# Performance work log

Measured on AMD Instinct MI355X. Metric: run time of the kernel, lower is better.

The kernel has to match this reference:

```python
import jax, jax.numpy as jnp
import numpy as np

N_NODES = 100000
N_EDGES = 1600000
IN, HID, OUT = 32, 32, 16


def setup_inputs() -> dict:
    key = jax.random.key(0)
    ks = jax.random.split(key, 8)
    return {
        "features": jax.random.normal(ks[0], (N_NODES, IN), dtype=jnp.float32),
        "src": jax.random.randint(ks[1], (N_EDGES,), 0, N_NODES, dtype=jnp.int32),
        "dst": jax.random.randint(ks[2], (N_EDGES,), 0, N_NODES, dtype=jnp.int32),
        "edge_weight": jax.random.uniform(ks[3], (N_EDGES,), dtype=jnp.float32),
        "W1": jax.random.normal(ks[4], (IN, HID), dtype=jnp.float32) * 0.1,
        "b1": jnp.zeros((HID,), dtype=jnp.float32),
        "W2": jax.random.normal(ks[5], (HID, OUT), dtype=jnp.float32) * 0.1,
        "b2": jnp.zeros((OUT,), dtype=jnp.float32),
    }


def _graph_conv(h, W, b, src, dst, edge_weight, norm_src, norm_dst, n):
    # DGL GraphConv, norm='both', with edge_weight (u_mul_e aggregation)
    h = h * norm_src[:, None]          # out-degree^-0.5 on source side
    h = h @ W                          # dense transform (tiny GEMM)
    m = h[src] * edge_weight[:, None]  # gather + edge weighting  [E, d]
    agg = jax.ops.segment_sum(m, dst, num_segments=n)  # scatter-add SpMM
    return agg * norm_dst[:, None] + b # in-degree^-0.5 + bias


def reference(features, src, dst, edge_weight, W1, b1, W2, b2):
    n = features.shape[0]
    ones_e = jnp.ones_like(edge_weight)
    deg_out = jnp.clip(jax.ops.segment_sum(ones_e, src, num_segments=n), 1.0)
    deg_in = jnp.clip(jax.ops.segment_sum(ones_e, dst, num_segments=n), 1.0)
    norm_src = deg_out ** -0.5
    norm_dst = deg_in ** -0.5
    h = _graph_conv(features, W1, b1, src, dst, edge_weight, norm_src, norm_dst, n)
    h = jax.nn.relu(h)
    # dropout is identity in eval mode
    h = _graph_conv(h, W2, b2, src, dst, edge_weight, norm_src, norm_dst, n)
    return h
```

## Files before the change

### kernel.cpp

```cpp
#include <hip/hip_runtime.h>
#include <hip/hip_fp16.h>


#define NB   391
#define CAPB 5504
#define EPB  4096

__device__ __forceinline__ long nt_load_i64(const long* p) {
    return __builtin_nontemporal_load(p);
}

__global__ __launch_bounds__(512) void partition_kernel(
        const int* __restrict__ src, const int* __restrict__ dst,
        const float* __restrict__ ew,
        int* __restrict__ g_cur_d, int* __restrict__ g_cur_s,
        int2* __restrict__ pack_part, unsigned char* __restrict__ src_part, int m) {
    __shared__ int hist_d[NB], hist_s[NB];
    __shared__ int lbase_d[NB], lbase_s[NB];
    __shared__ int gbase_d[NB], gbase_s[NB];
    __shared__ int cur_d[NB], cur_s[NB];
    __shared__ int sc[2][512];
    __shared__ long stage[EPB];
    __shared__ unsigned short dbuck[EPB];
    __shared__ unsigned char  sstage[EPB];
    __shared__ unsigned short sbuck[EPB];
    int t = threadIdx.x;
    for (int i = t; i < NB; i += 512) {
        hist_d[i] = 0; hist_s[i] = 0; cur_d[i] = 0; cur_s[i] = 0;
    }
    __syncthreads();
    int base_e = blockIdx.x * EPB;
    int total = m - base_e; if (total > EPB) total = EPB;
    int es[8], ed[8]; float wv[8];
#pragma unroll
    for (int k = 0; k < 8; k++) {
        int e = base_e + k * 512 + t;
        if (e < m) { es[k] = src[e]; ed[k] = dst[e]; wv[k] = ew[e]; }
        else ed[k] = -1;
    }
#pragma unroll
    for (int k = 0; k < 8; k++) {
        if (ed[k] >= 0) {
            atomicAdd(&hist_d[ed[k] >> 8], 1);
            atomicAdd(&hist_s[es[k] >> 8], 1);
        }
    }
    __syncthreads();
    if (t < 512) sc[0][t] = (t < NB) ? hist_d[t] : 0;
    __syncthreads();
    int pp = 0;
    for (int off = 1; off < 512; off <<= 1) {
        sc[1 - pp][t] = sc[pp][t] + (t >= off ? sc[pp][t - off] : 0);
        __syncthreads();
        pp ^= 1;
    }
    for (int i = t; i < NB; i += 512) lbase_d[i] = sc[pp][i] - hist_d[i];
    __syncthreads();
    sc[0][t] = (t < NB) ? hist_s[t] : 0;
    __syncthreads();
    pp = 0;
    for (int off = 1; off < 512; off <<= 1) {
        sc[1 - pp][t] = sc[pp][t] + (t >= off ? sc[pp][t - off] : 0);
        __syncthreads();
        pp ^= 1;
    }
    for (int i = t; i < NB; i += 512) lbase_s[i] = sc[pp][i] - hist_s[i];
    __syncthreads();
    for (int i = t; i < NB; i += 512) {
        int c = hist_d[i];
        gbase_d[i] = i * CAPB + (c ? atomicAdd(&g_cur_d[i], c) : 0);
        c = hist_s[i];
        gbase_s[i] = i * CAPB + (c ? atomicAdd(&g_cur_s[i], c) : 0);
    }
    __syncthreads();
#pragma unroll
    for (int k = 0; k < 8; k++) {
        if (ed[k] >= 0) {
            int d = ed[k], s = es[k];
            int bd = d >> 8;
            int r = atomicAdd(&cur_d[bd], 1);
            int pos = lbase_d[bd] + r;
            stage[pos] = (long)(unsigned int)(s | ((d & 255) << 20)) |
                         ((long)__float_as_int(wv[k]) << 32);
            dbuck[pos] = (unsigned short)bd;
            int bs = s >> 8;
            int rs = atomicAdd(&cur_s[bs], 1);
            int ps = lbase_s[bs] + rs;
            sstage[ps] = (unsigned char)(s & 255);
            sbuck[ps] = (unsigned short)bs;
        }
    }
    __syncthreads();
    long* packl = (long*)pack_part;
    for (int i = t; i < total; i += 512) {
        int b = dbuck[i];
        packl[(size_t)gbase_d[b] + (i - lbase_d[b])] = stage[i];
    }
    for (int i = t; i < total; i += 512) {
        int b = sbuck[i];
        src_part[(size_t)gbase_s[b] + (i - lbase_s[b])] = sstage[i];
    }
}

__global__ __launch_bounds__(1024) void csr_kernel(
                           const int2* __restrict__ pack_part,
                           const unsigned char* __restrict__ src_part,
                           const int* __restrict__ g_cur_d, const int* __restrict__ g_cur_s,
                           const float* __restrict__ feat, const float* __restrict__ W1,
                           int2* __restrict__ csr, int2* __restrict__ rs_cnt,
                           float* __restrict__ norm_src, float* __restrict__ norm_dst,
                           __half* __restrict__ h1, int n) {
    __shared__ int cnt[256];
    __shared__ int rowx[256];
    __shared__ int cur[256];
    __shared__ int cnt_s[256];
    __shared__ float nsrc[256];
    __shared__ float sW1[1024];
    extern __shared__ int2 stage[];
    int t = threadIdx.x, b = blockIdx.x;
    if (t < 256) { cnt[t] = 0; cur[t] = 0; cnt_s[t] = 0; }
    sW1[t] = W1[t];
    __syncthreads();
    int count = g_cur_d[b]; if (count > CAPB) count = CAPB;
    int count_s = g_cur_s[b]; if (count_s > CAPB) count_s = CAPB;
    const int2* p = pack_part + (size_t)b * CAPB;
    const unsigned char* sp = src_part + (size_t)b * CAPB;
    for (int e = t; e < count; e += 1024) atomicAdd(&cnt[p[e].x >> 20], 1);
    for (int e = t; e < count_s; e += 1024) atomicAdd(&cnt_s[sp[e]], 1);
    __syncthreads();
    if (t < 256) {
        int node = b * 256 + t;
        if (node < n) {
            int cs = cnt_s[t];
            float ns = rsqrtf((float)(cs > 1 ? cs : 1));
            nsrc[t] = ns;
            norm_src[node] = ns;
        } else nsrc[t] = 0.0f;
    }
    int c0 = 0;
    if (t < 256) { c0 = cnt[t]; rowx[t] = c0; }
    __syncthreads();
    for (int off = 1; off < 256; off <<= 1) {
        int v = 0;
        if (t < 256 && t >= off) v = rowx[t - off];
        __syncthreads();
        if (t < 256) rowx[t] += v;
        __syncthreads();
    }
    if (t < 256) {
        int excl = rowx[t] - c0;
        rowx[t] = excl;
        int node = b * 256 + t;
        if (node < n) {
            rs_cnt[node] = make_int2(b * CAPB + excl, c0);
            norm_dst[node] = rsqrtf((float)(c0 > 1 ? c0 : 1));
        }
    }
    __syncthreads();
    for (int e = t; e < count; e += 1024) {
        int2 v = p[e];
        int dl = v.x >> 20;
        int r = atomicAdd(&cur[dl], 1);
        stage[rowx[dl] + r] = make_int2(v.x & 0x1FFFF, v.y);
    }
    __syncthreads();
    int2* outp = csr + (size_t)b * CAPB;
    for (int e = t; e < count; e += 1024) outp[e] = stage[e];
    __syncthreads();
    float* sF = (float*)stage;
    int node0 = b * 256;
    int lim = n - node0; if (lim > 256) lim = 256; if (lim < 0) lim = 0;
    for (int o = t; o < lim * 32; o += 1024) {
        int i = o >> 5, k = o & 31;
        sF[o] = feat[(size_t)(node0 + i) * 32 + k] * nsrc[i];
    }
    __syncthreads();
    for (int o = t; o < lim * 32; o += 1024) {
        int i = o >> 5, col = o & 31;
        float acc = 0.0f;
#pragma unroll
        for (int k = 0; k < 32; k++) acc += sF[i * 32 + k] * sW1[k * 32 + col];
        h1[(size_t)(node0 + i) * 32 + col] = __float2half(acc);
    }
}

__global__ void gather1_fused_kernel(const __half* __restrict__ h1, const int2* __restrict__ csr,
                                     const int2* __restrict__ rs_cnt,
                                     const float* __restrict__ norm_src, const float* __restrict__ norm_dst,
                                     const float* __restrict__ W2, const float* __restrict__ b1,
                                     __half* __restrict__ h2, int n) {
    __shared__ float sW2[32 * 16];
    __shared__ float sB1[32];
    __shared__ float sX[4][8][32];
    int t = threadIdx.x;
    for (int i = t; i < 512; i += 256) sW2[i] = W2[i];
    if (t < 32) sB1[t] = b1[t];
    __syncthreads();
    int w = t >> 6, lane = t & 63;
    int q = lane >> 3;
    int dq = lane & 7;
    int node = (blockIdx.x * 4 + w) * 8 + q;
    bool valid = node < n;
    int2 rc = valid ? rs_cnt[node] : make_int2(0, 0);
    long base = rc.x;
    int c = rc.y;
    const float2* tv = (const float2*)h1;
    const long* csrl = (const long*)csr;
    float a00=0,a01=0,a02=0,a03=0, a10=0,a11=0,a12=0,a13=0;
    float a20=0,a21=0,a22=0,a23=0, a30=0,a31=0,a32=0,a33=0;
    int j = 0;
    for (; j + 3 < c; j += 4) {
        long q0 = nt_load_i64(csrl + base + j);
        long q1 = nt_load_i64(csrl + base + j + 1);
        long q2 = nt_load_i64(csrl + base + j + 2);
        long q3 = nt_load_i64(csrl + base + j + 3);
        float2 r0 = tv[(size_t)((int)q0 & 0xFFFFF) * 8 + dq];
        float2 r1 = tv[(size_t)((int)q1 & 0xFFFFF) * 8 + dq];
        float2 r2 = tv[(size_t)((int)q2 & 0xFFFFF) * 8 + dq];
        float2 r3 = tv[(size_t)((int)q3 & 0xFFFFF) * 8 + dq];
        float w0 = __int_as_float((int)(q0 >> 32)), w1 = __int_as_float((int)(q1 >> 32));
        float w2 = __int_as_float((int)(q2 >> 32)), w3 = __int_as_float((int)(q3 >> 32));
        float2 l0 = __half22float2(*(__half2*)&r0.x), h0 = __half22float2(*(__half2*)&r0.y);
        float2 l1 = __half22float2(*(__half2*)&r1.x), h1v = __half22float2(*(__half2*)&r1.y);
        float2 l2 = __half22float2(*(__half2*)&r2.x), h2v = __half22float2(*(__half2*)&r2.y);
        float2 l3 = __half22float2(*(__half2*)&r3.x), h3v = __half22float2(*(__half2*)&r3.y);
        a00 += l0.x * w0; a01 += l0.y * w0; a02 += h0.x * w0; a03 += h0.y * w0;
        a10 += l1.x * w1; a11 += l1.y * w1; a12 += h1v.x * w1; a13 += h1v.y * w1;
        a20 += l2.x * w2; a21 += l2.y * w2; a22 += h2v.x * w2; a23 += h2v.y * w2;
        a30 += l3.x * w3; a31 += l3.y * w3; a32 += h3v.x * w3; a33 += h3v.y * w3;
    }
    for (; j < c; j++) {
        long qq = nt_load_i64(csrl + base + j);
        float2 r = tv[(size_t)((int)qq & 0xFFFFF) * 8 + dq];
        float ww = __int_as_float((int)(qq >> 32));
        float2 l = __half22float2(*(__half2*)&r.x), h = __half22float2(*(__half2*)&r.y);
        a00 += l.x * ww; a01 += l.y * ww; a02 += h.x * ww; a03 += h.y * ww;
    }
    float s0 = (a00 + a10) + (a20 + a30);
    float s1 = (a01 + a11) + (a21 + a31);
    float s2 = (a02 + a12) + (a22 + a32);
    float s3 = (a03 + a13) + (a23 + a33);
    if (valid) {
        float nd = norm_dst[node], ns = norm_src[node];
        int d0 = 4 * dq;
        sX[w][q][d0]     = fmaxf(s0 * nd + sB1[d0],     0.0f) * ns;
        sX[w][q][d0 + 1] = fmaxf(s1 * nd + sB1[d0 + 1], 0.0f) * ns;
        sX[w][q][d0 + 2] = fmaxf(s2 * nd + sB1[d0 + 2], 0.0f) * ns;
        sX[w][q][d0 + 3] = fmaxf(s3 * nd + sB1[d0 + 3], 0.0f) * ns;
    }
    if (valid) {
        float o0 = 0.0f, o1 = 0.0f;
        int c0 = 2 * dq, c1 = 2 * dq + 1;
#pragma unroll
        for (int k = 0; k < 32; k++) {
            float x = sX[w][q][k];
            o0 += x * sW2[k * 16 + c0];
            o1 += x * sW2[k * 16 + c1];
        }
        ((__half2*)h2)[(size_t)node * 8 + dq] = __floats2half2_rn(o0, o1);
    }
}

__global__ void gather2_kernel(const __half* __restrict__ h2, const int2* __restrict__ csr,
                               const int2* __restrict__ rs_cnt,
                               const float* __restrict__ norm_dst, const float* __restrict__ b2,
                               float* __restrict__ out, int n) {
    int t = threadIdx.x;
    int w = t >> 6, lane = t & 63;
    int q = lane >> 2;
    int dq = lane & 3;
    int node = (blockIdx.x * 4 + w) * 16 + q;
    bool valid = node < n;
    int2 rc = valid ? rs_cnt[node] : make_int2(0, 0);
    long base = rc.x;
    int c = rc.y;
    const float2* tv = (const float2*)h2;
    const long* csrl = (const long*)csr;
    float a00=0,a01=0,a02=0,a03=0, a10=0,a11=0,a12=0,a13=0;
    float a20=0,a21=0,a22=0,a23=0, a30=0,a31=0,a32=0,a33=0;
    int j = 0;
    for (; j + 3 < c; j += 4) {
        long q0 = nt_load_i64(csrl + base + j);
        long q1 = nt_load_i64(csrl + base + j + 1);
        long q2 = nt_load_i64(csrl + base + j + 2);
        long q3 = nt_load_i64(csrl + base + j + 3);
        float2 r0 = tv[(size_t)((int)q0 & 0xFFFFF) * 4 + dq];
        float2 r1 = tv[(size_t)((int)q1 & 0xFFFFF) * 4 + dq];
        float2 r2 = tv[(size_t)((int)q2 & 0xFFFFF) * 4 + dq];
        float2 r3 = tv[(size_t)((int)q3 & 0xFFFFF) * 4 + dq];
        float w0 = __int_as_float((int)(q0 >> 32)), w1 = __int_as_float((int)(q1 >> 32));
        float w2 = __int_as_float((int)(q2 >> 32)), w3 = __int_as_float((int)(q3 >> 32));
        float2 l0 = __half22float2(*(__half2*)&r0.x), h0 = __half22float2(*(__half2*)&r0.y);
        float2 l1 = __half22float2(*(__half2*)&r1.x), h1v = __half22float2(*(__half2*)&r1.y);
        float2 l2 = __half22float2(*(__half2*)&r2.x), h2v = __half22float2(*(__half2*)&r2.y);
        float2 l3 = __half22float2(*(__half2*)&r3.x), h3v = __half22float2(*(__half2*)&r3.y);
        a00 += l0.x * w0; a01 += l0.y * w0; a02 += h0.x * w0; a03 += h0.y * w0;
        a10 += l1.x * w1; a11 += l1.y * w1; a12 += h1v.x * w1; a13 += h1v.y * w1;
        a20 += l2.x * w2; a21 += l2.y * w2; a22 += h2v.x * w2; a23 += h2v.y * w2;
        a30 += l3.x * w3; a31 += l3.y * w3; a32 += h3v.x * w3; a33 += h3v.y * w3;
    }
    for (; j < c; j++) {
        long qq = nt_load_i64(csrl + base + j);
        float2 r = tv[(size_t)((int)qq & 0xFFFFF) * 4 + dq];
        float ww = __int_as_float((int)(qq >> 32));
        float2 l = __half22float2(*(__half2*)&r.x), h = __half22float2(*(__half2*)&r.y);
        a00 += l.x * ww; a01 += l.y * ww; a02 += h.x * ww; a03 += h.y * ww;
    }
    if (valid) {
        float nd = norm_dst[node];
        int d0 = 4 * dq;
        float4 o;
        o.x = ((a00 + a10) + (a20 + a30)) * nd + b2[d0];
        o.y = ((a01 + a11) + (a21 + a31)) * nd + b2[d0 + 1];
        o.z = ((a02 + a12) + (a22 + a32)) * nd + b2[d0 + 2];
        o.w = ((a03 + a13) + (a23 + a33)) * nd + b2[d0 + 3];
        ((float4*)out)[(size_t)node * 4 + dq] = o;
    }
}

extern "C" void kernel_launch(void* const* d_in, const int* in_sizes, int n_in,
                              void* d_out, int out_size, void* d_ws, size_t ws_size,
                              hipStream_t stream) {
    const float* feat = (const float*)d_in[0];
    const int*   src  = (const int*)d_in[1];
    const int*   dst  = (const int*)d_in[2];
    const float* ew   = (const float*)d_in[3];
    const float* W1   = (const float*)d_in[4];
    const float* b1   = (const float*)d_in[5];
    const float* W2   = (const float*)d_in[6];
    const float* b2   = (const float*)d_in[7];
    float* out = (float*)d_out;

    const int n = in_sizes[0] / 32;
    const int m = in_sizes[1];

    char* wsb = (char*)d_ws;
    int2*   pack_part = (int2*)wsb;
    int2*   csr       = pack_part + (size_t)NB * CAPB;
    __half* h1        = (__half*)(csr + (size_t)NB * CAPB);
    __half* h2        = h1 + 32 * (size_t)n;
    float*  norm_src  = (float*)(h2 + 16 * (size_t)n);
    float*  norm_dst  = norm_src + n;
    int2*   rs_cnt    = (int2*)(norm_dst + n);
    int*    g_cur_d   = (int*)(rs_cnt + n);
    int*    g_cur_s   = g_cur_d + NB;
    unsigned char* src_part = (unsigned char*)(g_cur_s + NB);

    hipMemsetAsync(g_cur_d, 0, 2 * NB * sizeof(int), stream);

    partition_kernel<<<(m + EPB - 1) / EPB, 512, 0, stream>>>(src, dst, ew, g_cur_d, g_cur_s,
                                                              pack_part, src_part, m);
    csr_kernel<<<NB, 1024, CAPB * sizeof(int2), stream>>>(pack_part, src_part, g_cur_d, g_cur_s,
                                                          feat, W1, csr, rs_cnt,
                                                          norm_src, norm_dst, h1, n);
    gather1_fused_kernel<<<(n + 31) / 32, 256, 0, stream>>>(h1, csr, rs_cnt,
                                                            norm_src, norm_dst, W2, b1, h2, n);
    gather2_kernel<<<(n + 63) / 64, 256, 0, stream>>>(h2, csr, rs_cnt, norm_dst, b2, out, n);
}
```

Baseline: 186.9 us.

## Compute source degrees with global atomics and replace block scans with wave shuffles

Drops the second source-side bucket partition (histogram, scan, staging and the src_part scatter). Out-degrees are now counted with direct global atomicAdd into a per-node deg_src array, which csr_kernel reads. The shared-memory prefix scans are replaced with wavefront shuffle scans, csr_kernel keeps the first packed edges in registers instead of reading them twice, and the feature transform is vectorized with float4 loads, padded shared rows and half2 stores. The cost is 1.6M scattered global atomics and a larger memset covering n ints.

Measured after the change: 237.6 us. 27.2% more time.

```diff
diff --git a/kernel.cpp b/kernel.cpp
--- a/kernel.cpp
+++ b/kernel.cpp
@@ -13,21 +13,18 @@
 __global__ __launch_bounds__(512) void partition_kernel(
         const int* __restrict__ src, const int* __restrict__ dst,
         const float* __restrict__ ew,
-        int* __restrict__ g_cur_d, int* __restrict__ g_cur_s,
-        int2* __restrict__ pack_part, unsigned char* __restrict__ src_part, int m) {
-    __shared__ int hist_d[NB], hist_s[NB];
-    __shared__ int lbase_d[NB], lbase_s[NB];
-    __shared__ int gbase_d[NB], gbase_s[NB];
-    __shared__ int cur_d[NB], cur_s[NB];
-    __shared__ int sc[2][512];
+        int* __restrict__ g_cur_d, int* __restrict__ deg_src,
+        int2* __restrict__ pack_part, int m) {
+    __shared__ int hist_d[NB];
+    __shared__ int lbase_d[NB];
+    __shared__ int gbase_d[NB];
+    __shared__ int cur_d[NB];
+    __shared__ int woff[8];
     __shared__ long stage[EPB];
     __shared__ unsigned short dbuck[EPB];
-    __shared__ unsigned char  sstage[EPB];
-    __shared__ unsigned short sbuck[EPB];
     int t = threadIdx.x;
-    for (int i = t; i < NB; i += 512) {
-        hist_d[i] = 0; hist_s[i] = 0; cur_d[i] = 0; cur_s[i] = 0;
-    }
+    int lane = t & 63, w = t >> 6;
+    for (int i = t; i < NB; i += 512) { hist_d[i] = 0; cur_d[i] = 0; }
     __syncthreads();
     int base_e = blockIdx.x * EPB;
     int total = m - base_e; if (total > EPB) total = EPB;
@@ -42,35 +39,34 @@
     for (int k = 0; k < 8; k++) {
         if (ed[k] >= 0) {
             atomicAdd(&hist_d[ed[k] >> 8], 1);
-            atomicAdd(&hist_s[es[k] >> 8], 1);
-        }
-    }
-    __syncthreads();
-    if (t < 512) sc[0][t] = (t < NB) ? hist_d[t] : 0;
-    __syncthreads();
-    int pp = 0;
-    for (int off = 1; off < 512; off <<= 1) {
-        sc[1 - pp][t] = sc[pp][t] + (t >= off ? sc[pp][t - off] : 0);
-        __syncthreads();
-        pp ^= 1;
-    }
-    for (int i = t; i < NB; i += 512) lbase_d[i] = sc[pp][i] - hist_d[i];
-    __syncthreads();
-    sc[0][t] = (t < NB) ? hist_s[t] : 0;
-    __syncthreads();
-    pp = 0;
-    for (int off = 1; off < 512; off <<= 1) {
-        sc[1 - pp][t] = sc[pp][t] + (t >= off ? sc[pp][t - off] : 0);
-        __syncthreads();
-        pp ^= 1;
-    }
-    for (int i = t; i < NB; i += 512) lbase_s[i] = sc[pp][i] - hist_s[i];
-    __syncthreads();
+            atomicAdd(&deg_src[es[k]], 1);
+        }
+    }
+    __syncthreads();
+    int hv = (t < NB) ? hist_d[t] : 0;
+    int v = hv;
+#pragma unroll
+    for (int off = 1; off < 64; off <<= 1) {
+        int u = __shfl_up(v, off, 64);
+        if (lane >= off) v += u;
+    }
+    if (lane == 63) woff[w] = v;
+    __syncthreads();
+    if (t < 64) {
+        int s = (t < 8) ? woff[t] : 0;
+        int orig = s;
+#pragma unroll
+        for (int off = 1; off < 8; off <<= 1) {
+            int u = __shfl_up(s, off, 64);
+            if (lane >= off) s += u;
+        }
+        if (t < 8) woff[t] = s - orig;
+    }
+    __syncthreads();
+    if (t < NB) lbase_d[t] = v + woff[w] - hv;
     for (int i = t; i < NB; i += 512) {
         int c = hist_d[i];
         gbase_d[i] = i * CAPB + (c ? atomicAdd(&g_cur_d[i], c) : 0);
-        c = hist_s[i];
-        gbase_s[i] = i * CAPB + (c ? atomicAdd(&g_cur_s[i], c) : 0);
     }
     __syncthreads();
 #pragma unroll
@@ -83,11 +79,6 @@
             stage[pos] = (long)(unsigned int)(s | ((d & 255) << 20)) |
                          ((long)__float_as_int(wv[k]) << 32);
             dbuck[pos] = (unsigned short)bd;
-            int bs = s >> 8;
-            int rs = atomicAdd(&cur_s[bs], 1);
-            int ps = lbase_s[bs] + rs;
-            sstage[ps] = (unsigned char)(s & 255);
-            sbuck[ps] = (unsigned short)bs;
         }
     }
     __syncthreads();
@@ -96,16 +87,11 @@
         int b = dbuck[i];
         packl[(size_t)gbase_d[b] + (i - lbase_d[b])] = stage[i];
     }
-    for (int i = t; i < total; i += 512) {
-        int b = sbuck[i];
-        src_part[(size_t)gbase_s[b] + (i - lbase_s[b])] = sstage[i];
-    }
 }
 
 __global__ __launch_bounds__(1024) void csr_kernel(
                            const int2* __restrict__ pack_part,
-                           const unsigned char* __restrict__ src_part,
-                           const int* __restrict__ g_cur_d, const int* __restrict__ g_cur_s,
+                           const int* __restrict__ g_cur_d, const int* __restrict__ deg_src,
                            const float* __restrict__ feat, const float* __restrict__ W1,
                            int2* __restrict__ csr, int2* __restrict__ rs_cnt,
                            float* __restrict__ norm_src, float* __restrict__ norm_dst,
@@ -113,51 +99,65 @@
     __shared__ int cnt[256];
     __shared__ int rowx[256];
     __shared__ int cur[256];
-    __shared__ int cnt_s[256];
     __shared__ float nsrc[256];
     __shared__ float sW1[1024];
     extern __shared__ int2 stage[];
     int t = threadIdx.x, b = blockIdx.x;
-    if (t < 256) { cnt[t] = 0; cur[t] = 0; cnt_s[t] = 0; }
+    if (t < 256) { cnt[t] = 0; cur[t] = 0; }
     sW1[t] = W1[t];
     __syncthreads();
     int count = g_cur_d[b]; if (count > CAPB) count = CAPB;
-    int count_s = g_cur_s[b]; if (count_s > CAPB) count_s = CAPB;
     const int2* p = pack_part + (size_t)b * CAPB;
-    const unsigned char* sp = src_part + (size_t)b * CAPB;
-    for (int e = t; e < count; e += 1024) atomicAdd(&cnt[p[e].x >> 20], 1);
-    for (int e = t; e < count_s; e += 1024) atomicAdd(&cnt_s[sp[e]], 1);
-    __syncthreads();
+    int2 pk[4];
+#pragma unroll
+    for (int u = 0; u < 4; u++) {
+        int e = t + u * 1024;
+        if (e < count) { pk[u] = p[e]; atomicAdd(&cnt[pk[u].x >> 20], 1); }
+    }
+    for (int e = t + 4096; e < count; e += 1024)
+        atomicAdd(&cnt[p[e].x >> 20], 1);
+    __syncthreads();
+    if (t < 64) {
+        int c0 = cnt[t * 4], c1 = cnt[t * 4 + 1], c2 = cnt[t * 4 + 2], c3 = cnt[t * 4 + 3];
+        int tot = c0 + c1 + c2 + c3;
+        int incl = tot;
+#pragma unroll
+        for (int off = 1; off < 64; off <<= 1) {
+            int u = __shfl_up(incl, off, 64);
+            if (t >= off) incl += u;
+        }
+        int excl = incl - tot;
+        rowx[t * 4]     = excl;
+        rowx[t * 4 + 1] = excl + c0;
+        rowx[t * 4 + 2] = excl + c0 + c1;
+        rowx[t * 4 + 3] = excl + c0 + c1 + c2;
+    }
+    __syncthreads();
+    int node0 = b * 256;
     if (t < 256) {
-        int node = b * 256 + t;
+        int node = node0 + t;
         if (node < n) {
-            int cs = cnt_s[t];
-            float ns = rsqrtf((float)(cs > 1 ? cs : 1));
+            int c0 = cnt[t];
+            rs_cnt[node] = make_int2(b * CAPB + rowx[t], c0);
+            norm_dst[node] = rsqrtf((float)(c0 > 1 ? c0 : 1));
+            int ds = deg_src[node];
+            float ns = rsqrtf((float)(ds > 1 ? ds : 1));
             nsrc[t] = ns;
             norm_src[node] = ns;
         } else nsrc[t] = 0.0f;
     }
-    int c0 = 0;
-    if (t < 256) { c0 = cnt[t]; rowx[t] = c0; }
-    __syncthreads();
-    for (int off = 1; off < 256; off <<= 1) {
-        int v = 0;
-        if (t < 256 && t >= off) v = rowx[t - off];
-        __syncthreads();
-        if (t < 256) rowx[t] += v;
-        __syncthreads();
-    }
-    if (t < 256) {
-        int excl = rowx[t] - c0;
-        rowx[t] = excl;
-        int node = b * 256 + t;
-        if (node < n) {
-            rs_cnt[node] = make_int2(b * CAPB + excl, c0);
-            norm_dst[node] = rsqrtf((float)(c0 > 1 ? c0 : 1));
-        }
-    }
-    __syncthreads();
-    for (int e = t; e < count; e += 1024) {
+    __syncthreads();
+#pragma unroll
+    for (int u = 0; u < 4; u++) {
+        int e = t + u * 1024;
+        if (e < count) {
+            int2 v = pk[u];
+            int dl = v.x >> 20;
+            int r = atomicAdd(&cur[dl], 1);
+            stage[rowx[dl] + r] = make_int2(v.x & 0x1FFFF, v.y);
+        }
+    }
+    for (int e = t + 4096; e < count; e += 1024) {
         int2 v = p[e];
         int dl = v.x >> 20;
         int r = atomicAdd(&cur[dl], 1);
@@ -168,19 +168,27 @@
     for (int e = t; e < count; e += 1024) outp[e] = stage[e];
     __syncthreads();
     float* sF = (float*)stage;
-    int node0 = b * 256;
     int lim = n - node0; if (lim > 256) lim = 256; if (lim < 0) lim = 0;
-    for (int o = t; o < lim * 32; o += 1024) {
-        int i = o >> 5, k = o & 31;
-        sF[o] = feat[(size_t)(node0 + i) * 32 + k] * nsrc[i];
-    }
-    __syncthreads();
-    for (int o = t; o < lim * 32; o += 1024) {
-        int i = o >> 5, col = o & 31;
-        float acc = 0.0f;
-#pragma unroll
-        for (int k = 0; k < 32; k++) acc += sF[i * 32 + k] * sW1[k * 32 + col];
-        h1[(size_t)(node0 + i) * 32 + col] = __float2half(acc);
+    const float4* f4 = (const float4*)feat;
+    for (int o = t; o < lim * 8; o += 1024) {
+        int i = o >> 3, k4 = o & 7;
+        float4 vv = f4[(size_t)node0 * 8 + o];
+        float ns = nsrc[i];
+        vv.x *= ns; vv.y *= ns; vv.z *= ns; vv.w *= ns;
+        ((float4*)(sF + i * 36))[k4] = vv;
+    }
+    __syncthreads();
+    __half2* h1v = (__half2*)h1;
+    for (int o = t; o < lim * 16; o += 1024) {
+        int i = o >> 4, cp = o & 15;
+        float a0 = 0.0f, a1 = 0.0f;
+#pragma unroll
+        for (int k = 0; k < 32; k++) {
+            float x = sF[i * 36 + k];
+            a0 += x * sW1[k * 32 + 2 * cp];
+            a1 += x * sW1[k * 32 + 2 * cp + 1];
+        }
+        h1v[(size_t)(node0 + i) * 16 + cp] = __floats2half2_rn(a0, a1);
     }
 }
 
@@ -191,7 +199,7 @@
                                      __half* __restrict__ h2, int n) {
     __shared__ float sW2[32 * 16];
     __shared__ float sB1[32];
-    __shared__ float sX[4][8][32];
+    __shared__ float sX[4][8][33];
     int t = threadIdx.x;
     for (int i = t; i < 512; i += 256) sW2[i] = W2[i];
     if (t < 32) sB1[t] = b1[t];
@@ -343,14 +351,13 @@
     float*  norm_dst  = norm_src + n;
     int2*   rs_cnt    = (int2*)(norm_dst + n);
     int*    g_cur_d   = (int*)(rs_cnt + n);
-    int*    g_cur_s   = g_cur_d + NB;
-    unsigned char* src_part = (unsigned char*)(g_cur_s + NB);
-
-    hipMemsetAsync(g_cur_d, 0, 2 * NB * sizeof(int), stream);
-
-    partition_kernel<<<(m + EPB - 1) / EPB, 512, 0, stream>>>(src, dst, ew, g_cur_d, g_cur_s,
-                                                              pack_part, src_part, m);
-    csr_kernel<<<NB, 1024, CAPB * sizeof(int2), stream>>>(pack_part, src_part, g_cur_d, g_cur_s,
+    int*    deg_src   = g_cur_d + NB;
+
+    hipMemsetAsync(g_cur_d, 0, (NB + n) * sizeof(int), stream);
+
+    partition_kernel<<<(m + EPB - 1) / EPB, 512, 0, stream>>>(src, dst, ew, g_cur_d, deg_src,
+                                                              pack_part, m);
+    csr_kernel<<<NB, 1024, CAPB * sizeof(int2), stream>>>(pack_part, g_cur_d, deg_src,
                                                           feat, W1, csr, rs_cnt,
                                                           norm_src, norm_dst, h1, n);
     gather1_fused_kernel<<<(n + 31) / 32, 256, 0, stream>>>(h1, csr, rs_cnt,
```

## Replace CSR build and per-node gathers with bucketed LDS atomic accumulation

Applied to the files above, without the earlier changes.

Drops the per-bucket CSR sort. The two aggregation kernels now read the destination-bucketed edge partitions directly and accumulate each 256-node bucket in shared memory with float atomics. The degree-based norm_dst is computed inside the first gather, and the partition kernel's block scans are rewritten as wave shuffle scans. This removes the CSR write/read pass and the rs_cnt indirection, but only 391 blocks are launched and the many LDS atomics may contend on high-degree nodes.

New measurement: 637.9 us. 241% more time.

```diff
diff --git a/kernel.cpp b/kernel.cpp
--- a/kernel.cpp
+++ b/kernel.cpp
@@ -5,10 +5,6 @@
 #define NB   391
 #define CAPB 5504
 #define EPB  4096
-
-__device__ __forceinline__ long nt_load_i64(const long* p) {
-    return __builtin_nontemporal_load(p);
-}
 
 __global__ __launch_bounds__(512) void partition_kernel(
         const int* __restrict__ src, const int* __restrict__ dst,
@@ -19,12 +15,12 @@
     __shared__ int lbase_d[NB], lbase_s[NB];
     __shared__ int gbase_d[NB], gbase_s[NB];
     __shared__ int cur_d[NB], cur_s[NB];
-    __shared__ int sc[2][512];
+    __shared__ int woffd[8], woffs[8];
     __shared__ long stage[EPB];
     __shared__ unsigned short dbuck[EPB];
     __shared__ unsigned char  sstage[EPB];
     __shared__ unsigned short sbuck[EPB];
-    int t = threadIdx.x;
+    int t = threadIdx.x, lane = t & 63, w = t >> 6;
     for (int i = t; i < NB; i += 512) {
         hist_d[i] = 0; hist_s[i] = 0; cur_d[i] = 0; cur_s[i] = 0;
     }
@@ -46,26 +42,34 @@
         }
     }
     __syncthreads();
-    if (t < 512) sc[0][t] = (t < NB) ? hist_d[t] : 0;
-    __syncthreads();
-    int pp = 0;
-    for (int off = 1; off < 512; off <<= 1) {
-        sc[1 - pp][t] = sc[pp][t] + (t >= off ? sc[pp][t - off] : 0);
-        __syncthreads();
-        pp ^= 1;
-    }
-    for (int i = t; i < NB; i += 512) lbase_d[i] = sc[pp][i] - hist_d[i];
-    __syncthreads();
-    sc[0][t] = (t < NB) ? hist_s[t] : 0;
-    __syncthreads();
-    pp = 0;
-    for (int off = 1; off < 512; off <<= 1) {
-        sc[1 - pp][t] = sc[pp][t] + (t >= off ? sc[pp][t - off] : 0);
-        __syncthreads();
-        pp ^= 1;
-    }
-    for (int i = t; i < NB; i += 512) lbase_s[i] = sc[pp][i] - hist_s[i];
-    __syncthreads();
+    int hvd = (t < NB) ? hist_d[t] : 0;
+    int hvs = (t < NB) ? hist_s[t] : 0;
+    int vd = hvd, vs = hvs;
+#pragma unroll
+    for (int off = 1; off < 64; off <<= 1) {
+        int ud = __shfl_up(vd, off, 64);
+        int us = __shfl_up(vs, off, 64);
+        if (lane >= off) { vd += ud; vs += us; }
+    }
+    if (lane == 63) { woffd[w] = vd; woffs[w] = vs; }
+    __syncthreads();
+    if (t < 64) {
+        int sd = (t < 8) ? woffd[t] : 0;
+        int ss = (t < 8) ? woffs[t] : 0;
+        int od = sd, os = ss;
+#pragma unroll
+        for (int off = 1; off < 8; off <<= 1) {
+            int ud = __shfl_up(sd, off, 64);
+            int us = __shfl_up(ss, off, 64);
+            if (lane >= off) { sd += ud; ss += us; }
+        }
+        if (t < 8) { woffd[t] = sd - od; woffs[t] = ss - os; }
+    }
+    __syncthreads();
+    if (t < NB) {
+        lbase_d[t] = vd + woffd[w] - hvd;
+        lbase_s[t] = vs + woffs[w] - hvs;
+    }
     for (int i = t; i < NB; i += 512) {
         int c = hist_d[i];
         gbase_d[i] = i * CAPB + (c ? atomicAdd(&g_cur_d[i], c) : 0);
@@ -102,219 +106,172 @@
     }
 }
 
-__global__ __launch_bounds__(1024) void csr_kernel(
-                           const int2* __restrict__ pack_part,
-                           const unsigned char* __restrict__ src_part,
-                           const int* __restrict__ g_cur_d, const int* __restrict__ g_cur_s,
-                           const float* __restrict__ feat, const float* __restrict__ W1,
-                           int2* __restrict__ csr, int2* __restrict__ rs_cnt,
-                           float* __restrict__ norm_src, float* __restrict__ norm_dst,
-                           __half* __restrict__ h1, int n) {
-    __shared__ int cnt[256];
-    __shared__ int rowx[256];
-    __shared__ int cur[256];
+__global__ __launch_bounds__(1024) void transform1_kernel(
+        const unsigned char* __restrict__ src_part, const int* __restrict__ g_cur_s,
+        const float* __restrict__ feat, const float* __restrict__ W1,
+        float* __restrict__ norm_src, __half* __restrict__ h1, int n) {
     __shared__ int cnt_s[256];
     __shared__ float nsrc[256];
     __shared__ float sW1[1024];
-    extern __shared__ int2 stage[];
+    __shared__ __align__(16) float sF[256 * 36];
     int t = threadIdx.x, b = blockIdx.x;
-    if (t < 256) { cnt[t] = 0; cur[t] = 0; cnt_s[t] = 0; }
+    if (t < 256) cnt_s[t] = 0;
     sW1[t] = W1[t];
     __syncthreads();
-    int count = g_cur_d[b]; if (count > CAPB) count = CAPB;
     int count_s = g_cur_s[b]; if (count_s > CAPB) count_s = CAPB;
-    const int2* p = pack_part + (size_t)b * CAPB;
     const unsigned char* sp = src_part + (size_t)b * CAPB;
-    for (int e = t; e < count; e += 1024) atomicAdd(&cnt[p[e].x >> 20], 1);
     for (int e = t; e < count_s; e += 1024) atomicAdd(&cnt_s[sp[e]], 1);
     __syncthreads();
+    int node0 = b * 256;
     if (t < 256) {
-        int node = b * 256 + t;
+        int node = node0 + t;
         if (node < n) {
-            int cs = cnt_s[t];
-            float ns = rsqrtf((float)(cs > 1 ? cs : 1));
+            int ds = cnt_s[t];
+            float ns = rsqrtf((float)(ds > 1 ? ds : 1));
             nsrc[t] = ns;
             norm_src[node] = ns;
         } else nsrc[t] = 0.0f;
     }
-    int c0 = 0;
-    if (t < 256) { c0 = cnt[t]; rowx[t] = c0; }
-    __syncthreads();
-    for (int off = 1; off < 256; off <<= 1) {
-        int v = 0;
-        if (t < 256 && t >= off) v = rowx[t - off];
-        __syncthreads();
-        if (t < 256) rowx[t] += v;
-        __syncthreads();
-    }
-    if (t < 256) {
-        int excl = rowx[t] - c0;
-        rowx[t] = excl;
-        int node = b * 256 + t;
-        if (node < n) {
-            rs_cnt[node] = make_int2(b * CAPB + excl, c0);
-            norm_dst[node] = rsqrtf((float)(c0 > 1 ? c0 : 1));
-        }
-    }
-    __syncthreads();
-    for (int e = t; e < count; e += 1024) {
-        int2 v = p[e];
-        int dl = v.x >> 20;
-        int r = atomicAdd(&cur[dl], 1);
-        stage[rowx[dl] + r] = make_int2(v.x & 0x1FFFF, v.y);
-    }
-    __syncthreads();
-    int2* outp = csr + (size_t)b * CAPB;
-    for (int e = t; e < count; e += 1024) outp[e] = stage[e];
-    __syncthreads();
-    float* sF = (float*)stage;
+    __syncthreads();
+    int lim = n - node0; if (lim > 256) lim = 256; if (lim < 0) lim = 0;
+    const float4* f4 = (const float4*)feat;
+    for (int o = t; o < lim * 8; o += 1024) {
+        int i = o >> 3, k4 = o & 7;
+        float4 vv = f4[(size_t)node0 * 8 + o];
+        float ns = nsrc[i];
+        vv.x *= ns; vv.y *= ns; vv.z *= ns; vv.w *= ns;
+        ((float4*)(sF + i * 36))[k4] = vv;
+    }
+    __syncthreads();
+    __half2* h1v = (__half2*)h1;
+    for (int o = t; o < lim * 16; o += 1024) {
+        int i = o >> 4, cp = o & 15;
+        float a0 = 0.0f, a1 = 0.0f;
+#pragma unroll
+        for (int k = 0; k < 32; k++) {
+            float x = sF[i * 36 + k];
+            a0 += x * sW1[k * 32 + 2 * cp];
+            a1 += x * sW1[k * 32 + 2 * cp + 1];
+        }
+        h1v[(size_t)(node0 + i) * 16 + cp] = __floats2half2_rn(a0, a1);
+    }
+}
+
+__global__ __launch_bounds__(1024) void gather1_kernel(
+        const int2* __restrict__ pack_part, const int* __restrict__ g_cur_d,
+        const __half* __restrict__ h1, const float* __restrict__ norm_src,
+        const float* __restrict__ W2, const float* __restrict__ b1,
+        float* __restrict__ norm_dst, __half* __restrict__ h2, int n) {
+    __shared__ float acc[256 * 33];
+    __shared__ int cnt[256];
+    __shared__ float sW2[512];
+    __shared__ float sB1[32];
+    __shared__ float sndv[256], snsv[256];
+    int t = threadIdx.x, b = blockIdx.x;
+    for (int i = t; i < 256 * 33; i += 1024) acc[i] = 0.0f;
+    if (t < 256) cnt[t] = 0;
+    if (t < 512) sW2[t] = W2[t];
+    else if (t < 544) sB1[t - 512] = b1[t - 512];
+    __syncthreads();
+    int count = g_cur_d[b]; if (count > CAPB) count = CAPB;
+    const int2* p = pack_part + (size_t)b * CAPB;
+    const float4* h1f4 = (const float4*)h1;
+    int eq = t >> 2, q = t & 3;
+    for (int e0 = 0; e0 < count; e0 += 256) {
+        int e = e0 + eq;
+        if (e < count) {
+            int2 v = p[e];
+            int s  = v.x & 0x1FFFF;
+            int dl = (v.x >> 20) & 255;
+            float wgt = __int_as_float(v.y);
+            if (q == 0) atomicAdd(&cnt[dl], 1);
+            float4 r = h1f4[(size_t)s * 4 + q];
+            float* ap = acc + dl * 33 + 8 * q;
+            const __half2* hp = (const __half2*)&r;
+#pragma unroll
+            for (int j = 0; j < 4; j++) {
+                float2 f = __half22float2(hp[j]);
+                atomicAdd(ap + 2 * j,     f.x * wgt);
+                atomicAdd(ap + 2 * j + 1, f.y * wgt);
+            }
+        }
+    }
+    __syncthreads();
     int node0 = b * 256;
     int lim = n - node0; if (lim > 256) lim = 256; if (lim < 0) lim = 0;
+    if (t < 256) {
+        int c0 = cnt[t];
+        float nd = rsqrtf((float)(c0 > 1 ? c0 : 1));
+        sndv[t] = nd;
+        snsv[t] = (t < lim) ? norm_src[node0 + t] : 0.0f;
+        if (t < lim) norm_dst[node0 + t] = nd;
+    }
+    __syncthreads();
     for (int o = t; o < lim * 32; o += 1024) {
         int i = o >> 5, k = o & 31;
-        sF[o] = feat[(size_t)(node0 + i) * 32 + k] * nsrc[i];
-    }
-    __syncthreads();
-    for (int o = t; o < lim * 32; o += 1024) {
-        int i = o >> 5, col = o & 31;
-        float acc = 0.0f;
-#pragma unroll
-        for (int k = 0; k < 32; k++) acc += sF[i * 32 + k] * sW1[k * 32 + col];
-        h1[(size_t)(node0 + i) * 32 + col] = __float2half(acc);
-    }
-}
-
-__global__ void gather1_fused_kernel(const __half* __restrict__ h1, const int2* __restrict__ csr,
-                                     const int2* __restrict__ rs_cnt,
-                                     const float* __restrict__ norm_src, const float* __restrict__ norm_dst,
-                                     const float* __restrict__ W2, const float* __restrict__ b1,
-                                     __half* __restrict__ h2, int n) {
-    __shared__ float sW2[32 * 16];
-    __shared__ float sB1[32];
-    __shared__ float sX[4][8][32];
-    int t = threadIdx.x;
-    for (int i = t; i < 512; i += 256) sW2[i] = W2[i];
-    if (t < 32) sB1[t] = b1[t];
-    __syncthreads();
-    int w = t >> 6, lane = t & 63;
-    int q = lane >> 3;
-    int dq = lane & 7;
-    int node = (blockIdx.x * 4 + w) * 8 + q;
-    bool valid = node < n;
-    int2 rc = valid ? rs_cnt[node] : make_int2(0, 0);
-    long base = rc.x;
-    int c = rc.y;
-    const float2* tv = (const float2*)h1;
-    const long* csrl = (const long*)csr;
-    float a00=0,a01=0,a02=0,a03=0, a10=0,a11=0,a12=0,a13=0;
-    float a20=0,a21=0,a22=0,a23=0, a30=0,a31=0,a32=0,a33=0;
-    int j = 0;
-    for (; j + 3 < c; j += 4) {
-        long q0 = nt_load_i64(csrl + base + j);
-        long q1 = nt_load_i64(csrl + base + j + 1);
-        long q2 = nt_load_i64(csrl + base + j + 2);
-        long q3 = nt_load_i64(csrl + base + j + 3);
-        float2 r0 = tv[(size_t)((int)q0 & 0xFFFFF) * 8 + dq];
-        float2 r1 = tv[(size_t)((int)q1 & 0xFFFFF) * 8 + dq];
-        float2 r2 = tv[(size_t)((int)q2 & 0xFFFFF) * 8 + dq];
-        float2 r3 = tv[(size_t)((int)q3 & 0xFFFFF) * 8 + dq];
-        float w0 = __int_as_float((int)(q0 >> 32)), w1 = __int_as_float((int)(q1 >> 32));
-        float w2 = __int_as_float((int)(q2 >> 32)), w3 = __int_as_float((int)(q3 >> 32));
-        float2 l0 = __half22float2(*(__half2*)&r0.x), h0 = __half22float2(*(__half2*)&r0.y);
-        float2 l1 = __half22float2(*(__half2*)&r1.x), h1v = __half22float2(*(__half2*)&r1.y);
-        float2 l2 = __half22float2(*(__half2*)&r2.x), h2v = __half22float2(*(__half2*)&r2.y);
-        float2 l3 = __half22float2(*(__half2*)&r3.x), h3v = __half22float2(*(__half2*)&r3.y);
-        a00 += l0.x * w0; a01 += l0.y * w0; a02 += h0.x * w0; a03 += h0.y * w0;
-        a10 += l1.x * w1; a11 += l1.y * w1; a12 += h1v.x * w1; a13 += h1v.y * w1;
-        a20 += l2.x * w2; a21 += l2.y * w2; a22 += h2v.x * w2; a23 += h2v.y * w2;
-        a30 += l3.x * w3; a31 += l3.y * w3; a32 += h3v.x * w3; a33 += h3v.y * w3;
-    }
-    for (; j < c; j++) {
-        long qq = nt_load_i64(csrl + base + j);
-        float2 r = tv[(size_t)((int)qq & 0xFFFFF) * 8 + dq];
-        float ww = __int_as_float((int)(qq >> 32));
-        float2 l = __half22float2(*(__half2*)&r.x), h = __half22float2(*(__half2*)&r.y);
-        a00 += l.x * ww; a01 += l.y * ww; a02 += h.x * ww; a03 += h.y * ww;
-    }
-    float s0 = (a00 + a10) + (a20 + a30);
-    float s1 = (a01 + a11) + (a21 + a31);
-    float s2 = (a02 + a12) + (a22 + a32);
-    float s3 = (a03 + a13) + (a23 + a33);
-    if (valid) {
-        float nd = norm_dst[node], ns = norm_src[node];
-        int d0 = 4 * dq;
-        sX[w][q][d0]     = fmaxf(s0 * nd + sB1[d0],     0.0f) * ns;
-        sX[w][q][d0 + 1] = fmaxf(s1 * nd + sB1[d0 + 1], 0.0f) * ns;
-        sX[w][q][d0 + 2] = fmaxf(s2 * nd + sB1[d0 + 2], 0.0f) * ns;
-        sX[w][q][d0 + 3] = fmaxf(s3 * nd + sB1[d0 + 3], 0.0f) * ns;
-    }
-    if (valid) {
-        float o0 = 0.0f, o1 = 0.0f;
-        int c0 = 2 * dq, c1 = 2 * dq + 1;
+        float x = fmaxf(acc[i * 33 + k] * sndv[i] + sB1[k], 0.0f) * snsv[i];
+        acc[i * 33 + k] = x;
+    }
+    __syncthreads();
+    __half2* h2v = (__half2*)h2;
+    for (int o = t; o < lim * 8; o += 1024) {
+        int i = o >> 3, cp = o & 7;
+        float a0 = 0.0f, a1 = 0.0f;
 #pragma unroll
         for (int k = 0; k < 32; k++) {
-            float x = sX[w][q][k];
-            o0 += x * sW2[k * 16 + c0];
-            o1 += x * sW2[k * 16 + c1];
-        }
-        ((__half2*)h2)[(size_t)node * 8 + dq] = __floats2half2_rn(o0, o1);
-    }
-}
-
-__global__ void gather2_kernel(const __half* __restrict__ h2, const int2* __restrict__ csr,
-                               const int2* __restrict__ rs_cnt,
-                               const float* __restrict__ norm_dst, const float* __restrict__ b2,
-                               float* __restrict__ out, int n) {
-    int t = threadIdx.x;
-    int w = t >> 6, lane = t & 63;
-    int q = lane >> 2;
-    int dq = lane & 3;
-    int node = (blockIdx.x * 4 + w) * 16 + q;
-    bool valid = node < n;
-    int2 rc = valid ? rs_cnt[node] : make_int2(0, 0);
-    long base = rc.x;
-    int c = rc.y;
-    const float2* tv = (const float2*)h2;
-    const long* csrl = (const long*)csr;
-    float a00=0,a01=0,a02=0,a03=0, a10=0,a11=0,a12=0,a13=0;
-    float a20=0,a21=0,a22=0,a23=0, a30=0,a31=0,a32=0,a33=0;
-    int j = 0;
-    for (; j + 3 < c; j += 4) {
-        long q0 = nt_load_i64(csrl + base + j);
-        long q1 = nt_load_i64(csrl + base + j + 1);
-        long q2 = nt_load_i64(csrl + base + j + 2);
-        long q3 = nt_load_i64(csrl + base + j + 3);
-        float2 r0 = tv[(size_t)((int)q0 & 0xFFFFF) * 4 + dq];
-        float2 r1 = tv[(size_t)((int)q1 & 0xFFFFF) * 4 + dq];
-        float2 r2 = tv[(size_t)((int)q2 & 0xFFFFF) * 4 + dq];
-        float2 r3 = tv[(size_t)((int)q3 & 0xFFFFF) * 4 + dq];
-        float w0 = __int_as_float((int)(q0 >> 32)), w1 = __int_as_float((int)(q1 >> 32));
-        float w2 = __int_as_float((int)(q2 >> 32)), w3 = __int_as_float((int)(q3 >> 32));
-        float2 l0 = __half22float2(*(__half2*)&r0.x), h0 = __half22float2(*(__half2*)&r0.y);
-        float2 l1 = __half22float2(*(__half2*)&r1.x), h1v = __half22float2(*(__half2*)&r1.y);
-        float2 l2 = __half22float2(*(__half2*)&r2.x), h2v = __half22float2(*(__half2*)&r2.y);
-        float2 l3 = __half22float2(*(__half2*)&r3.x), h3v = __half22float2(*(__half2*)&r3.y);
-        a00 += l0.x * w0; a01 += l0.y * w0; a02 += h0.x * w0; a03 += h0.y * w0;
-        a10 += l1.x * w1; a11 += l1.y * w1; a12 += h1v.x * w1; a13 += h1v.y * w1;
-        a20 += l2.x * w2; a21 += l2.y * w2; a22 += h2v.x * w2; a23 += h2v.y * w2;
-        a30 += l3.x * w3; a31 += l3.y * w3; a32 += h3v.x * w3; a33 += h3v.y * w3;
-    }
-    for (; j < c; j++) {
-        long qq = nt_load_i64(csrl + base + j);
-        float2 r = tv[(size_t)((int)qq & 0xFFFFF) * 4 + dq];
-        float ww = __int_as_float((int)(qq >> 32));
-        float2 l = __half22float2(*(__half2*)&r.x), h = __half22float2(*(__half2*)&r.y);
-        a00 += l.x * ww; a01 += l.y * ww; a02 += h.x * ww; a03 += h.y * ww;
-    }
-    if (valid) {
-        float nd = norm_dst[node];
-        int d0 = 4 * dq;
-        float4 o;
-        o.x = ((a00 + a10) + (a20 + a30)) * nd + b2[d0];
-        o.y = ((a01 + a11) + (a21 + a31)) * nd + b2[d0 + 1];
-        o.z = ((a02 + a12) + (a22 + a32)) * nd + b2[d0 + 2];
-        o.w = ((a03 + a13) + (a23 + a33)) * nd + b2[d0 + 3];
-        ((float4*)out)[(size_t)node * 4 + dq] = o;
+            float x = acc[i * 33 + k];
+            a0 += x * sW2[k * 16 + 2 * cp];
+            a1 += x * sW2[k * 16 + 2 * cp + 1];
+        }
+        h2v[(size_t)(node0 + i) * 8 + cp] = __floats2half2_rn(a0, a1);
+    }
+}
+
+__global__ __launch_bounds__(1024) void gather2_kernel(
+        const int2* __restrict__ pack_part, const int* __restrict__ g_cur_d,
+        const __half* __restrict__ h2, const float* __restrict__ norm_dst,
+        const float* __restrict__ b2, float* __restrict__ out, int n) {
+    __shared__ __align__(16) float acc[256 * 20];
+    __shared__ float sB2[16];
+    int t = threadIdx.x, b = blockIdx.x;
+    for (int i = t; i < 256 * 20; i += 1024) acc[i] = 0.0f;
+    if (t < 16) sB2[t] = b2[t];
+    __syncthreads();
+    int count = g_cur_d[b]; if (count > CAPB) count = CAPB;
+    const int2* p = pack_part + (size_t)b * CAPB;
+    const float4* h2f4 = (const float4*)h2;
+    int eq = t >> 1, q = t & 1;
+    for (int e0 = 0; e0 < count; e0 += 512) {
+        int e = e0 + eq;
+        if (e < count) {
+            int2 v = p[e];
+            int s  = v.x & 0x1FFFF;
+            int dl = (v.x >> 20) & 255;
+            float wgt = __int_as_float(v.y);
+            float4 r = h2f4[(size_t)s * 2 + q];
+            float* ap = acc + dl * 20 + 8 * q;
+            const __half2* hp = (const __half2*)&r;
+#pragma unroll
+            for (int j = 0; j < 4; j++) {
+                float2 f = __half22float2(hp[j]);
+                atomicAdd(ap + 2 * j,     f.x * wgt);
+                atomicAdd(ap + 2 * j + 1, f.y * wgt);
+            }
+        }
+    }
+    __syncthreads();
+    int node0 = b * 256;
+    int lim = n - node0; if (lim > 256) lim = 256; if (lim < 0) lim = 0;
+    float4* out4 = (float4*)out;
+    for (int o = t; o < lim * 4; o += 1024) {
+        int i = o >> 2, q2 = o & 3;
+        float nd = norm_dst[node0 + i];
+        float4 a = *(const float4*)(acc + i * 20 + 4 * q2);
+        a.x = a.x * nd + sB2[4 * q2];
+        a.y = a.y * nd + sB2[4 * q2 + 1];
+        a.z = a.z * nd + sB2[4 * q2 + 2];
+        a.w = a.w * nd + sB2[4 * q2 + 3];
+        out4[(size_t)(node0 + i) * 4 + q2] = a;
     }
 }
 
@@ -336,13 +293,11 @@
 
     char* wsb = (char*)d_ws;
     int2*   pack_part = (int2*)wsb;
-    int2*   csr       = pack_part + (size_t)NB * CAPB;
-    __half* h1        = (__half*)(csr + (size_t)NB * CAPB);
+    __half* h1        = (__half*)(pack_part + (size_t)NB * CAPB);
     __half* h2        = h1 + 32 * (size_t)n;
     float*  norm_src  = (float*)(h2 + 16 * (size_t)n);
     float*  norm_dst  = norm_src + n;
-    int2*   rs_cnt    = (int2*)(norm_dst + n);
-    int*    g_cur_d   = (int*)(rs_cnt + n);
+    int*    g_cur_d   = (int*)(norm_dst + n);
     int*    g_cur_s   = g_cur_d + NB;
     unsigned char* src_part = (unsigned char*)(g_cur_s + NB);
 
@@ -350,10 +305,8 @@
 
     partition_kernel<<<(m + EPB - 1) / EPB, 512, 0, stream>>>(src, dst, ew, g_cur_d, g_cur_s,
                                                               pack_part, src_part, m);
-    csr_kernel<<<NB, 1024, CAPB * sizeof(int2), stream>>>(pack_part, src_part, g_cur_d, g_cur_s,
-                                                          feat, W1, csr, rs_cnt,
-                                                          norm_src, norm_dst, h1, n);
-    gather1_fused_kernel<<<(n + 31) / 32, 256, 0, stream>>>(h1, csr, rs_cnt,
-                                                            norm_src, norm_dst, W2, b1, h2, n);
-    gather2_kernel<<<(n + 63) / 64, 256, 0, stream>>>(h2, csr, rs_cnt, norm_dst, b2, out, n);
-}
+    transform1_kernel<<<NB, 1024, 0, stream>>>(src_part, g_cur_s, feat, W1, norm_src, h1, n);
+    gather1_kernel<<<NB, 1024, 0, stream>>>(pack_part, g_cur_d, h1, norm_src, W2, b1,
+                                            norm_dst, h2, n);
+    gather2_kernel<<<NB, 1024, 0, stream>>>(pack_part, g_cur_d, h2, norm_dst, b2, out, n);
+}
```
